# Kernel optimization log

Hardware: AMD Instinct MI355X
Metric: run time of the kernel (lower is better)

## Reference

```python
import jax, jax.numpy as jnp
import numpy as np

KS = 3
PAD = 1
N = KS * KS  # 9 sampling points per output location


def setup_inputs() -> dict:
    key = jax.random.key(0)
    k1, k2, k3 = jax.random.split(key, 3)
    b, c, H, W, outc = 4, 128, 64, 64, 128
    x = jax.random.normal(k1, (b, c, H, W), jnp.float32)
    offset = jax.random.normal(k2, (b, 2 * N, H, W), jnp.float32)
    weight = jax.random.normal(k3, (outc, c, KS, KS), jnp.float32) * 0.05
    return {"x": x, "offset": offset, "weight": weight}


def reference(x, offset, weight):
    b, c, H, W = x.shape
    h, w = offset.shape[2], offset.shape[3]
    # reorder interleaved (x,y,x,y,...) offset channels to (all x, all y)
    idx = jnp.concatenate([jnp.arange(0, 2 * N, 2), jnp.arange(1, 2 * N, 2)])
    offset = offset[:, idx]
    # zero padding
    xp = jnp.pad(x, ((0, 0), (0, 0), (PAD, PAD), (PAD, PAD)))
    Hp, Wp = H + 2 * PAD, W + 2 * PAD
    # kernel-relative offsets p_n: [1, 2N, 1, 1]
    r = np.arange(-(KS - 1) // 2, (KS - 1) // 2 + 1)
    pnx, pny = np.meshgrid(r, r, indexing='ij')
    p_n = jnp.asarray(np.concatenate([pnx.flatten(), pny.flatten()]).reshape(1, 2 * N, 1, 1), jnp.float32)
    # base grid p_0: [1, 2N, h, w], coords start at 1 (padded frame)
    p0x, p0y = np.meshgrid(np.arange(1, h + 1), np.arange(1, w + 1), indexing='ij')
    p_0 = jnp.asarray(np.concatenate([np.tile(p0x.reshape(1, 1, h, w), (1, N, 1, 1)),
                                      np.tile(p0y.reshape(1, 1, h, w), (1, N, 1, 1))], axis=1), jnp.float32)
    p = jnp.transpose(p_0 + p_n + offset, (0, 2, 3, 1))  # [b, h, w, 2N]
    px, py = p[..., :N], p[..., N:]
    fx, fy = jnp.floor(px), jnp.floor(py)
    # 4 corner integer coords, clamped to padded image
    q_lt_x = jnp.clip(fx, 0, Hp - 1).astype(jnp.int32)
    q_lt_y = jnp.clip(fy, 0, Wp - 1).astype(jnp.int32)
    q_rb_x = jnp.clip(fx + 1, 0, Hp - 1).astype(jnp.int32)
    q_rb_y = jnp.clip(fy + 1, 0, Wp - 1).astype(jnp.int32)
    # out-of-range mask: snap p to floor(p) there (matches original, incl. zero grad thru floor)
    mask_x = jax.lax.stop_gradient(((px < PAD) | (px > Hp - 1 - PAD)).astype(px.dtype))
    mask_y = jax.lax.stop_gradient(((py < PAD) | (py > Wp - 1 - PAD)).astype(py.dtype))
    px = px * (1 - mask_x) + fx * mask_x
    py = py * (1 - mask_y) + fy * mask_y
    px = jnp.clip(px, 0, Hp - 1)
    py = jnp.clip(py, 0, Wp - 1)
    qltx = q_lt_x.astype(px.dtype); qlty = q_lt_y.astype(px.dtype)
    qrbx = q_rb_x.astype(px.dtype); qrby = q_rb_y.astype(px.dtype)
    # bilinear weights: [b, h, w, N]
    g_lt = (1 + (qltx - px)) * (1 + (qlty - py))
    g_rb = (1 - (qrbx - px)) * (1 - (qrby - py))
    g_lb = (1 + (qltx - px)) * (1 - (qrby - py))
    g_rt = (1 - (qrbx - px)) * (1 + (qlty - py))

    xv = xp.reshape(b, c, Hp * Wp)

    def gather(qx, qy):
        lin = (qx * Wp + qy).reshape(b, 1, h * w * N)
        g = jnp.take_along_axis(xv, jnp.broadcast_to(lin, (b, c, h * w * N)), axis=2)
        return g.reshape(b, c, h, w, N)

    x_off = (g_lt[:, None] * gather(q_lt_x, q_lt_y)
             + g_rb[:, None] * gather(q_rb_x, q_rb_y)
             + g_lb[:, None] * gather(q_lt_x, q_rb_y)
             + g_rt[:, None] * gather(q_rb_x, q_lt_y))  # [b, c, h, w, N]
    # N = i*ks + j -> out[(h,i),(w,j)]
    xo = x_off.reshape(b, c, h, w, KS, KS).transpose(0, 1, 2, 4, 3, 5).reshape(b, c, h * KS, w * KS)
    out = jax.lax.conv_general_dilated(xo, weight, window_strides=(KS, KS), padding='VALID',
                                       dimension_numbers=('NCHW', 'OIHW', 'NCHW'))
    return out
```

## Files before the change

kernel.cpp:

```cpp
#include <hip/hip_runtime.h>


typedef __bf16  v8bf16 __attribute__((ext_vector_type(8)));
typedef __bf16  bf16x2 __attribute__((ext_vector_type(2)));
typedef float   f32x4  __attribute__((ext_vector_type(4)));
typedef float   f32x16 __attribute__((ext_vector_type(16)));
typedef unsigned short ushort4v __attribute__((ext_vector_type(4)));
typedef _Float16 half4v __attribute__((ext_vector_type(4)));

#define CIN  128
#define NPT  9
#define KTOT 1152
#define OC   128
#define PX   32
#define NDESC (NPT * PX)
#define KSTEPS 36
#define KSC  12
#define LDBc 392
#define KS32 72
#define KSC32 24
#define LDR32 392

#define PB_WFRAG 72
#define PB_XPOSE 1024
#define PB_TOTAL (PB_WFRAG + PB_XPOSE)

__device__ __forceinline__ uint4 desc_make(const float* __restrict__ off,
                                           int b, int i, int j, int tap) {
    float ox = off[(((b * 18) + 2 * tap) << 12) + (i << 6) + j];
    float oy = off[(((b * 18) + 2 * tap + 1) << 12) + (i << 6) + j];
    float px = (float)(i + tap / 3) + ox;
    float py = (float)(j + tap % 3) + oy;
    float fx = floorf(px), fy = floorf(py);
    int qltx = (int)fminf(fmaxf(fx, 0.f), 65.f);
    int qlty = (int)fminf(fmaxf(fy, 0.f), 65.f);
    int qrbx = (int)fminf(fmaxf(fx + 1.f, 0.f), 65.f);
    int qrby = (int)fminf(fmaxf(fy + 1.f, 0.f), 65.f);
    if (px < 1.f || px > 64.f) px = fx;
    if (py < 1.f || py > 64.f) py = fy;
    px = fminf(fmaxf(px, 0.f), 65.f);
    py = fminf(fmaxf(py, 0.f), 65.f);
    float wxl = 1.f + (float)qltx - px;
    float wxr = 1.f - ((float)qrbx - px);
    float wyl = 1.f + (float)qlty - py;
    float wyr = 1.f - ((float)qrby - py);
    float g[4] = { wxl * wyl, wxr * wyr, wxl * wyr, wxr * wyl };
    int qx[4] = { qltx, qrbx, qltx, qrbx };
    int qy[4] = { qlty, qrby, qrby, qlty };
    unsigned short idx[4];
    half4v gh;
    #pragma unroll
    for (int cr = 0; cr < 4; ++cr) {
        bool inb = (qx[cr] >= 1) && (qx[cr] <= 64) && (qy[cr] >= 1) && (qy[cr] <= 64);
        idx[cr] = inb ? (unsigned short)((qx[cr] - 1) * 64 + (qy[cr] - 1)) : 0;
        gh[cr]  = inb ? (_Float16)g[cr] : (_Float16)0.f;
    }
    uint4 rec;
    rec.x = (unsigned)idx[0] | ((unsigned)idx[1] << 16);
    rec.y = (unsigned)idx[2] | ((unsigned)idx[3] << 16);
    __builtin_memcpy(&rec.z, &gh, 8);
    return rec;
}

__global__ __launch_bounds__(256) void prep_kernel(
    const float* __restrict__ x, const float* __restrict__ w,
    __bf16* __restrict__ wfrag, __bf16* __restrict__ xt)
{
    __shared__ float tile[64][33];
    const int bid = blockIdx.x;
    const int tid = threadIdx.x;

    if (bid < PB_WFRAG) {
        int t = bid * 256 + tid;
        int lane = t & 63;
        int ks   = (t >> 6) % KS32;
        int ot4  = t / (KS32 * 64);
        int o    = ot4 * 32 + (lane & 31);
        v8bf16 frag;
        #pragma unroll
        for (int e = 0; e < 8; ++e) {
            int k   = ks * 16 + ((lane >> 5) * 8) + e;
            int tap = k >> 7, c = k & 127;
            frag[e] = (__bf16)w[(size_t)o * KTOT + c * NPT + tap];
        }
        *(v8bf16*)(wfrag + (size_t)t * 8) = frag;
    } else {
        const int bidx = bid - PB_WFRAG;
        const int b   = bidx >> 8;
        const int hw0 = ((bidx >> 2) & 63) * 64;
        const int c0  = (bidx & 3) * 32;
        #pragma unroll
        for (int r = 0; r < 8; ++r) {
            int c_l  = (tid >> 6) + r * 4;
            int hw_l = tid & 63;
            tile[hw_l][c_l] = x[((size_t)(b * CIN + c0 + c_l) << 12) + hw0 + hw_l];
        }
        __syncthreads();
        #pragma unroll
        for (int r = 0; r < 8; ++r) {
            int hw_l = (tid >> 5) + r * 8;
            int c_l  = tid & 31;
            xt[((size_t)(b * 4096 + hw0 + hw_l)) * CIN + c0 + c_l] = (__bf16)tile[hw_l][c_l];
        }
    }
}

__global__ __launch_bounds__(256) void fullk_kernel(
    const float* __restrict__ off, const __bf16* __restrict__ xt,
    const __bf16* __restrict__ wfrag, float* __restrict__ out)
{
    __shared__ __align__(16) __bf16 Bt[PX][LDR32];
    __shared__ __align__(16) uint4 sDesc[NDESC];

    const int bidx = blockIdx.x;
    const int b    = (bidx & 7) >> 1;
    const int sub  = ((bidx >> 3) << 1) | (bidx & 1);
    const int i    = sub >> 1;
    const int j0   = (sub & 1) * PX;
    const int tid  = threadIdx.x;

    const int l  = tid & 63;
    const int wv = tid >> 6;

    const __bf16* xtb = xt + (((size_t)b << 12) * CIN);

    {
        sDesc[tid] = desc_make(off, b, i, j0 + (tid & 31), tid >> 5);
        if (tid < 32) sDesc[256 + tid] = desc_make(off, b, i, j0 + tid, 8);
    }
    __syncthreads();

    f32x16 acc = {0.f,0.f,0.f,0.f,0.f,0.f,0.f,0.f,0.f,0.f,0.f,0.f,0.f,0.f,0.f,0.f};
    const __bf16* brow  = &Bt[l & 31][(l >> 5) * 8];
    const __bf16* warow = wfrag + (((size_t)wv * KS32) * 64 + l) * 8;

    const int q  = l >> 4;
    const int ll = l & 15;
    const __bf16* gbase = xtb + 8 * ll;

    for (int t = 0; t < 3; ++t) {
        {
            uint4 qd[6];
            int   pp[6], tt[6];
            #pragma unroll
            for (int m = 0; m < 6; ++m) {
                int dl = wv * 24 + m * 4 + q;
                tt[m] = dl >> 5;
                pp[m] = dl & 31;
                qd[m] = sDesc[t * 96 + dl];
            }

            #pragma unroll
            for (int h = 0; h < 2; ++h) {
                uint4  v[3][4];
                half4v gh[3];
                #pragma unroll
                for (int m = 0; m < 3; ++m) {
                    uint4 qm = qd[h * 3 + m];
                    unsigned int zz[2] = { qm.z, qm.w };
                    __builtin_memcpy(&gh[m], &zz, 8);
                    unsigned short idx[4] = {
                        (unsigned short)(qm.x & 0xffff), (unsigned short)(qm.x >> 16),
                        (unsigned short)(qm.y & 0xffff), (unsigned short)(qm.y >> 16) };
                    #pragma unroll
                    for (int cr = 0; cr < 4; ++cr)
                        v[m][cr] = *(const uint4*)(gbase + (size_t)idx[cr] * CIN);
                }
                #pragma unroll
                for (int m = 0; m < 3; ++m) {
                    float s[8] = {0.f,0.f,0.f,0.f,0.f,0.f,0.f,0.f};
                    #pragma unroll
                    for (int cr = 0; cr < 4; ++cr) {
                        float gf = (float)gh[m][cr];
                        unsigned int dw[4] = { v[m][cr].x, v[m][cr].y, v[m][cr].z, v[m][cr].w };
                        #pragma unroll
                        for (int e = 0; e < 4; ++e) {
                            float clo, chi;
                            unsigned int lo = dw[e] << 16, hi = dw[e] & 0xffff0000u;
                            __builtin_memcpy(&clo, &lo, 4);
                            __builtin_memcpy(&chi, &hi, 4);
                            s[2 * e]     += gf * clo;
                            s[2 * e + 1] += gf * chi;
                        }
                    }
                    v8bf16 pr;
                    #pragma unroll
                    for (int e = 0; e < 8; ++e) pr[e] = (__bf16)s[e];
                    int mm = h * 3 + m;
                    *(v8bf16*)&Bt[pp[mm]][tt[mm] * CIN + 8 * ll] = pr;
                }
            }
        }
        __syncthreads();

        #pragma unroll 6
        for (int ks = 0; ks < KSC32; ++ks) {
            v8bf16 afrag = *(const v8bf16*)(warow + (size_t)(t * KSC32 + ks) * 64 * 8);
            v8bf16 bfrag = *(const v8bf16*)(brow + ks * 16);
            acc = __builtin_amdgcn_mfma_f32_32x32x16_bf16(afrag, bfrag, acc, 0, 0, 0);
        }
        if (t < 2) __syncthreads();
    }

    {
        int obase = wv * 32 + 4 * (l >> 5);
        float* opb = out + (((size_t)(b * OC + obase)) << 12) + (i << 6) + j0 + (l & 31);
        #pragma unroll
        for (int reg = 0; reg < 16; ++reg) {
            int oo = (reg & 3) + 8 * (reg >> 2);
            opb[(size_t)oo << 12] = acc[reg];
        }
    }
}

__global__ __launch_bounds__(512, 8) void deform_fused_kernel(
    const float* __restrict__ x, const float* __restrict__ off,
    const float* __restrict__ w, const __bf16* __restrict__ wfrag,
    const __bf16* __restrict__ xt, float* __restrict__ out, int mode)
{
    __shared__ __align__(16) __bf16 Bt[PX][LDBc];
    __shared__ __align__(8)  unsigned short sIdxP[NDESC][4];
    __shared__ __align__(8)  _Float16      sGP[NDESC][4];

    const int bidx = blockIdx.x;
    const int b   = bidx >> 8;
    const int i   = (bidx >> 2) & 63;
    const int j0  = ((bidx >> 1) & 1) * PX;
    const int oh  = bidx & 1;
    const int tid = threadIdx.x;

    if (tid < NDESC) {
        int k = tid >> 5, p = tid & 31;
        int j = j0 + p;
        float ox = off[(((b * 18) + 2 * k) * 64 + i) * 64 + j];
        float oy = off[(((b * 18) + 2 * k + 1) * 64 + i) * 64 + j];
        float px = (float)(i + k / 3) + ox;
        float py = (float)(j + k % 3) + oy;
        float fx = floorf(px), fy = floorf(py);
        int qltx = (int)fminf(fmaxf(fx, 0.f), 65.f);
        int qlty = (int)fminf(fmaxf(fy, 0.f), 65.f);
        int qrbx = (int)fminf(fmaxf(fx + 1.f, 0.f), 65.f);
        int qrby = (int)fminf(fmaxf(fy + 1.f, 0.f), 65.f);
        if (px < 1.f || px > 64.f) px = fx;
        if (py < 1.f || py > 64.f) py = fy;
        px = fminf(fmaxf(px, 0.f), 65.f);
        py = fminf(fmaxf(py, 0.f), 65.f);
        float wxl = 1.f + (float)qltx - px;
        float wxr = 1.f - ((float)qrbx - px);
        float wyl = 1.f + (float)qlty - py;
        float wyr = 1.f - ((float)qrby - py);
        float g[4] = { wxl * wyl, wxr * wyr, wxl * wyr, wxr * wyl };
        int qx[4] = { qltx, qrbx, qltx, qrbx };
        int qy[4] = { qlty, qrby, qrby, qlty };
        #pragma unroll
        for (int cr = 0; cr < 4; ++cr) {
            bool inb = (qx[cr] >= 1) && (qx[cr] <= 64) && (qy[cr] >= 1) && (qy[cr] <= 64);
            sIdxP[tid][cr] = inb ? (unsigned short)((qx[cr] - 1) * 64 + (qy[cr] - 1)) : 0;
            sGP[tid][cr]   = inb ? (_Float16)g[cr] : (_Float16)0.f;
        }
    }
    __syncthreads();

    const int l    = tid & 63;
    const int wv   = tid >> 6;
    const int ot   = oh * 4 + (wv & 3);
    const int ph   = wv >> 2;
    const int quad = l >> 4;
    const int lr   = l & 15;

    f32x4 acc = {0.f, 0.f, 0.f, 0.f};
    const __bf16* xtb = xt + ((size_t)b * 4096) * CIN;
    const float*  xb  = x + ((size_t)b * CIN << 12);
    const __bf16* brow = &Bt[ph * 16 + lr][quad * 8];

    for (int t = 0; t < 3; ++t) {
        if (mode == 2) {
            #pragma unroll 4
            for (int dd = 0; dd < KSC; ++dd) {
                int dl = wv * KSC + dd;
                int tap_l = dl >> 5, p = dl & 31;
                int d = t * 96 + dl;
                ushort4v id = *(const ushort4v*)&sIdxP[d][0];
                half4v   gh = *(const half4v*)&sGP[d][0];
                float s0 = 0.f, s1 = 0.f;
                #pragma unroll
                for (int cr = 0; cr < 4; ++cr) {
                    unsigned int v = *(const unsigned int*)(xtb + (size_t)id[cr] * CIN + 2 * l);
                    float c0v, c1v;
                    unsigned int lo = v << 16, hi = v & 0xffff0000u;
                    __builtin_memcpy(&c0v, &lo, 4);
                    __builtin_memcpy(&c1v, &hi, 4);
                    float gf = (float)gh[cr];
                    s0 += gf * c0v;
                    s1 += gf * c1v;
                }
                bf16x2 pr = { (__bf16)s0, (__bf16)s1 };
                *(bf16x2*)&Bt[p][tap_l * CIN + 2 * l] = pr;
            }
        } else {
            for (int dd = 0; dd < KSC; ++dd) {
                int dl = wv * KSC + dd;
                int tap_l = dl >> 5, p = dl & 31;
                int d = t * 96 + dl;
                ushort4v id = *(const ushort4v*)&sIdxP[d][0];
                half4v   gh = *(const half4v*)&sGP[d][0];
                float s0 = 0.f, s1 = 0.f;
                #pragma unroll
                for (int cr = 0; cr < 4; ++cr) {
                    float gf = (float)gh[cr];
                    s0 += gf * xb[((size_t)(2 * l) << 12) + id[cr]];
                    s1 += gf * xb[((size_t)(2 * l + 1) << 12) + id[cr]];
                }
                bf16x2 pr = { (__bf16)s0, (__bf16)s1 };
                *(bf16x2*)&Bt[p][tap_l * CIN + 2 * l] = pr;
            }
        }
        __syncthreads();

        #pragma unroll 4
        for (int ks = 0; ks < KSC; ++ks) {
            int ks_g = t * KSC + ks;
            v8bf16 bfrag = *(const v8bf16*)(brow + ks * 32);
            v8bf16 afrag;
            if (mode >= 1) {
                afrag = *(const v8bf16*)(wfrag + (((size_t)ot * KSTEPS + ks_g) * 64 + l) * 8);
            } else {
                int o = ot * 16 + lr;
                #pragma unroll
                for (int e = 0; e < 8; ++e) {
                    int k = ks_g * 32 + quad * 8 + e;
                    int tap = k >> 7, c = k & 127;
                    afrag[e] = (__bf16)w[(size_t)o * KTOT + c * NPT + tap];
                }
            }
            acc = __builtin_amdgcn_mfma_f32_16x16x32_bf16(afrag, bfrag, acc, 0, 0, 0);
        }
        if (t < 2) __syncthreads();
    }

    {
        int obase = ot * 16 + quad * 4;
        float* op = out + (((size_t)(b * OC + obase)) << 12) + (i << 6) + j0 + ph * 16 + lr;
        #pragma unroll
        for (int r = 0; r < 4; ++r)
            op[(size_t)r << 12] = acc[r];
    }
}

__global__ __launch_bounds__(256) void wfrag_kernel(const float* __restrict__ w,
                                                    __bf16* __restrict__ wfrag) {
    int t = blockIdx.x * 256 + threadIdx.x;
    if (t >= 8 * KSTEPS * 64) return;
    int lane = t & 63;
    int ks   = (t >> 6) % KSTEPS;
    int ot   = t / (KSTEPS * 64);
    int o    = ot * 16 + (lane & 15);
    v8bf16 frag;
    #pragma unroll
    for (int e = 0; e < 8; ++e) {
        int k   = ks * 32 + (lane >> 4) * 8 + e;
        int tap = k >> 7, c = k & 127;
        frag[e] = (__bf16)w[(size_t)o * KTOT + c * NPT + tap];
    }
    *(v8bf16*)(wfrag + (size_t)t * 8) = frag;
}

__global__ __launch_bounds__(256) void xpose_kernel(const float* __restrict__ x,
                                                    __bf16* __restrict__ xt) {
    __shared__ float tile[64][33];
    const int bidx = blockIdx.x;
    const int b   = bidx >> 8;
    const int hw0 = ((bidx >> 2) & 63) * 64;
    const int c0  = (bidx & 3) * 32;
    const int tid = threadIdx.x;
    #pragma unroll
    for (int r = 0; r < 8; ++r) {
        int c_l  = (tid >> 6) + r * 4;
        int hw_l = tid & 63;
        tile[hw_l][c_l] = x[((size_t)(b * CIN + c0 + c_l) << 12) + hw0 + hw_l];
    }
    __syncthreads();
    #pragma unroll
    for (int r = 0; r < 8; ++r) {
        int hw_l = (tid >> 5) + r * 8;
        int c_l  = tid & 31;
        xt[((size_t)(b * 4096 + hw0 + hw_l)) * CIN + c0 + c_l] = (__bf16)tile[hw_l][c_l];
    }
}

extern "C" void kernel_launch(void* const* d_in, const int* in_sizes, int n_in,
                              void* d_out, int out_size, void* d_ws, size_t ws_size,
                              hipStream_t stream) {
    const float* x   = (const float*)d_in[0];
    const float* off = (const float*)d_in[1];
    const float* w   = (const float*)d_in[2];
    float* out = (float*)d_out;

    const size_t wfrag_bytes = (size_t)OC * KTOT * sizeof(__bf16);
    const size_t xt_bytes    = (size_t)4 * 4096 * CIN * sizeof(__bf16);

    int mode = 0;
    if (ws_size >= wfrag_bytes + xt_bytes) mode = 3;
    else if (ws_size >= wfrag_bytes) mode = 1;

    __bf16* wfrag = (__bf16*)d_ws;
    __bf16* xt    = (__bf16*)((char*)d_ws + wfrag_bytes);

    if (mode == 3) {
        prep_kernel<<<PB_TOTAL, 256, 0, stream>>>(x, w, wfrag, xt);
        fullk_kernel<<<512, 256, 0, stream>>>(off, xt, wfrag, out);
    } else {
        if (mode >= 1)
            wfrag_kernel<<<(8 * KSTEPS * 64 + 255) / 256, 256, 0, stream>>>(w, wfrag);
        deform_fused_kernel<<<4 * 64 * 2 * 2, 512, 0, stream>>>(x, off, w, wfrag, xt, out, mode);
    }
}
```

Before: 84.75 us.

## Switch fullk path to fp16 with packed-half blend and double-buffered B tile

Converts the prepared weights and transposed input to fp16 and uses fp16 MFMA. The bilinear blend now runs as packed half8 multiply-adds instead of unpacking bf16 to fp32. The B tile in shared memory is double-buffered, so the gather for the next tap group is issued before the MFMA loop on the current one, and launch bounds now request 2 blocks per CU. Accumulating the blend in fp16 lowers precision and risks overflow relative to fp32 accumulation, and the doubled shared memory buffer may limit occupancy.

Measured after the change: 83.88 us, median of 2. Within noise of the previous version (-1.0%).

```diff
diff --git a/kernel.cpp b/kernel.cpp
--- a/kernel.cpp
+++ b/kernel.cpp
@@ -7,6 +7,7 @@
 typedef float   f32x16 __attribute__((ext_vector_type(16)));
 typedef unsigned short ushort4v __attribute__((ext_vector_type(4)));
 typedef _Float16 half4v __attribute__((ext_vector_type(4)));
+typedef _Float16 half8  __attribute__((ext_vector_type(8)));
 
 #define CIN  128
 #define NPT  9
@@ -64,7 +65,7 @@
 
 __global__ __launch_bounds__(256) void prep_kernel(
     const float* __restrict__ x, const float* __restrict__ w,
-    __bf16* __restrict__ wfrag, __bf16* __restrict__ xt)
+    _Float16* __restrict__ wfrag, _Float16* __restrict__ xt)
 {
     __shared__ float tile[64][33];
     const int bid = blockIdx.x;
@@ -76,14 +77,14 @@
         int ks   = (t >> 6) % KS32;
         int ot4  = t / (KS32 * 64);
         int o    = ot4 * 32 + (lane & 31);
-        v8bf16 frag;
+        half8 frag;
         #pragma unroll
         for (int e = 0; e < 8; ++e) {
             int k   = ks * 16 + ((lane >> 5) * 8) + e;
             int tap = k >> 7, c = k & 127;
-            frag[e] = (__bf16)w[(size_t)o * KTOT + c * NPT + tap];
-        }
-        *(v8bf16*)(wfrag + (size_t)t * 8) = frag;
+            frag[e] = (_Float16)w[(size_t)o * KTOT + c * NPT + tap];
+        }
+        *(half8*)(wfrag + (size_t)t * 8) = frag;
     } else {
         const int bidx = bid - PB_WFRAG;
         const int b   = bidx >> 8;
@@ -100,16 +101,16 @@
         for (int r = 0; r < 8; ++r) {
             int hw_l = (tid >> 5) + r * 8;
             int c_l  = tid & 31;
-            xt[((size_t)(b * 4096 + hw0 + hw_l)) * CIN + c0 + c_l] = (__bf16)tile[hw_l][c_l];
-        }
-    }
-}
-
-__global__ __launch_bounds__(256) void fullk_kernel(
-    const float* __restrict__ off, const __bf16* __restrict__ xt,
-    const __bf16* __restrict__ wfrag, float* __restrict__ out)
+            xt[((size_t)(b * 4096 + hw0 + hw_l)) * CIN + c0 + c_l] = (_Float16)tile[hw_l][c_l];
+        }
+    }
+}
+
+__global__ __launch_bounds__(256, 2) void fullk_kernel(
+    const float* __restrict__ off, const _Float16* __restrict__ xt,
+    const _Float16* __restrict__ wfrag, float* __restrict__ out)
 {
-    __shared__ __align__(16) __bf16 Bt[PX][LDR32];
+    __shared__ __align__(16) _Float16 Bt[2][PX][LDR32];
     __shared__ __align__(16) uint4 sDesc[NDESC];
 
     const int bidx = blockIdx.x;
@@ -122,7 +123,7 @@
     const int l  = tid & 63;
     const int wv = tid >> 6;
 
-    const __bf16* xtb = xt + (((size_t)b << 12) * CIN);
+    const _Float16* xtb = xt + (((size_t)b << 12) * CIN);
 
     {
         sDesc[tid] = desc_make(off, b, i, j0 + (tid & 31), tid >> 5);
@@ -131,73 +132,65 @@
     __syncthreads();
 
     f32x16 acc = {0.f,0.f,0.f,0.f,0.f,0.f,0.f,0.f,0.f,0.f,0.f,0.f,0.f,0.f,0.f,0.f};
-    const __bf16* brow  = &Bt[l & 31][(l >> 5) * 8];
-    const __bf16* warow = wfrag + (((size_t)wv * KS32) * 64 + l) * 8;
+    const _Float16* warow = wfrag + (((size_t)wv * KS32) * 64 + l) * 8;
 
     const int q  = l >> 4;
     const int ll = l & 15;
-    const __bf16* gbase = xtb + 8 * ll;
+    const _Float16* gbase = xtb + 8 * ll;
+
+    auto stage = [&](int t, _Float16 (*B)[LDR32]) {
+        uint4 qd[6];
+        int   pp[6], tt[6];
+        #pragma unroll
+        for (int m = 0; m < 6; ++m) {
+            int dl = wv * 24 + m * 4 + q;
+            tt[m] = dl >> 5;
+            pp[m] = dl & 31;
+            qd[m] = sDesc[t * 96 + dl];
+        }
+        #pragma unroll
+        for (int h = 0; h < 2; ++h) {
+            uint4  v[3][4];
+            half4v gh[3];
+            #pragma unroll
+            for (int m = 0; m < 3; ++m) {
+                uint4 qm = qd[h * 3 + m];
+                unsigned int zz[2] = { qm.z, qm.w };
+                __builtin_memcpy(&gh[m], &zz, 8);
+                unsigned short idx[4] = {
+                    (unsigned short)(qm.x & 0xffff), (unsigned short)(qm.x >> 16),
+                    (unsigned short)(qm.y & 0xffff), (unsigned short)(qm.y >> 16) };
+                #pragma unroll
+                for (int cr = 0; cr < 4; ++cr)
+                    v[m][cr] = *(const uint4*)(gbase + (size_t)idx[cr] * CIN);
+            }
+            #pragma unroll
+            for (int m = 0; m < 3; ++m) {
+                half8 s = {0, 0, 0, 0, 0, 0, 0, 0};
+                #pragma unroll
+                for (int cr = 0; cr < 4; ++cr) {
+                    half8 vh;
+                    __builtin_memcpy(&vh, &v[m][cr], 16);
+                    s += vh * gh[m][cr];
+                }
+                int mm = h * 3 + m;
+                *(half8*)&B[pp[mm]][tt[mm] * CIN + 8 * ll] = s;
+            }
+        }
+    };
+
+    stage(0, Bt[0]);
+    __syncthreads();
 
     for (int t = 0; t < 3; ++t) {
-        {
-            uint4 qd[6];
-            int   pp[6], tt[6];
-            #pragma unroll
-            for (int m = 0; m < 6; ++m) {
-                int dl = wv * 24 + m * 4 + q;
-                tt[m] = dl >> 5;
-                pp[m] = dl & 31;
-                qd[m] = sDesc[t * 96 + dl];
-            }
-
-            #pragma unroll
-            for (int h = 0; h < 2; ++h) {
-                uint4  v[3][4];
-                half4v gh[3];
-                #pragma unroll
-                for (int m = 0; m < 3; ++m) {
-                    uint4 qm = qd[h * 3 + m];
-                    unsigned int zz[2] = { qm.z, qm.w };
-                    __builtin_memcpy(&gh[m], &zz, 8);
-                    unsigned short idx[4] = {
-                        (unsigned short)(qm.x & 0xffff), (unsigned short)(qm.x >> 16),
-                        (unsigned short)(qm.y & 0xffff), (unsigned short)(qm.y >> 16) };
-                    #pragma unroll
-                    for (int cr = 0; cr < 4; ++cr)
-                        v[m][cr] = *(const uint4*)(gbase + (size_t)idx[cr] * CIN);
-                }
-                #pragma unroll
-                for (int m = 0; m < 3; ++m) {
-                    float s[8] = {0.f,0.f,0.f,0.f,0.f,0.f,0.f,0.f};
-                    #pragma unroll
-                    for (int cr = 0; cr < 4; ++cr) {
-                        float gf = (float)gh[m][cr];
-                        unsigned int dw[4] = { v[m][cr].x, v[m][cr].y, v[m][cr].z, v[m][cr].w };
-                        #pragma unroll
-                        for (int e = 0; e < 4; ++e) {
-                            float clo, chi;
-                            unsigned int lo = dw[e] << 16, hi = dw[e] & 0xffff0000u;
-                            __builtin_memcpy(&clo, &lo, 4);
-                            __builtin_memcpy(&chi, &hi, 4);
-                            s[2 * e]     += gf * clo;
-                            s[2 * e + 1] += gf * chi;
-                        }
-                    }
-                    v8bf16 pr;
-                    #pragma unroll
-                    for (int e = 0; e < 8; ++e) pr[e] = (__bf16)s[e];
-                    int mm = h * 3 + m;
-                    *(v8bf16*)&Bt[pp[mm]][tt[mm] * CIN + 8 * ll] = pr;
-                }
-            }
-        }
-        __syncthreads();
-
+        if (t < 2) stage(t + 1, Bt[(t + 1) & 1]);
+
+        const _Float16* brow = &Bt[t & 1][l & 31][(l >> 5) * 8];
         #pragma unroll 6
         for (int ks = 0; ks < KSC32; ++ks) {
-            v8bf16 afrag = *(const v8bf16*)(warow + (size_t)(t * KSC32 + ks) * 64 * 8);
-            v8bf16 bfrag = *(const v8bf16*)(brow + ks * 16);
-            acc = __builtin_amdgcn_mfma_f32_32x32x16_bf16(afrag, bfrag, acc, 0, 0, 0);
+            half8 afrag = *(const half8*)(warow + (size_t)(t * KSC32 + ks) * 64 * 8);
+            half8 bfrag = *(const half8*)(brow + ks * 16);
+            acc = __builtin_amdgcn_mfma_f32_32x32x16_f16(afrag, bfrag, acc, 0, 0, 0);
         }
         if (t < 2) __syncthreads();
     }
@@ -396,20 +389,21 @@
     const float* w   = (const float*)d_in[2];
     float* out = (float*)d_out;
 
-    const size_t wfrag_bytes = (size_t)OC * KTOT * sizeof(__bf16);
-    const size_t xt_bytes    = (size_t)4 * 4096 * CIN * sizeof(__bf16);
+    const size_t wfrag_bytes = (size_t)OC * KTOT * 2;
+    const size_t xt_bytes    = (size_t)4 * 4096 * CIN * 2;
 
     int mode = 0;
     if (ws_size >= wfrag_bytes + xt_bytes) mode = 3;
     else if (ws_size >= wfrag_bytes) mode = 1;
 
-    __bf16* wfrag = (__bf16*)d_ws;
-    __bf16* xt    = (__bf16*)((char*)d_ws + wfrag_bytes);
-
     if (mode == 3) {
+        _Float16* wfrag = (_Float16*)d_ws;
+        _Float16* xt    = (_Float16*)((char*)d_ws + wfrag_bytes);
         prep_kernel<<<PB_TOTAL, 256, 0, stream>>>(x, w, wfrag, xt);
         fullk_kernel<<<512, 256, 0, stream>>>(off, xt, wfrag, out);
     } else {
+        __bf16* wfrag = (__bf16*)d_ws;
+        __bf16* xt    = (__bf16*)((char*)d_ws + wfrag_bytes);
         if (mode >= 1)
             wfrag_kernel<<<(8 * KSTEPS * 64 + 255) / 256, 256, 0, stream>>>(w, wfrag);
         deform_fused_kernel<<<4 * 64 * 2 * 2, 512, 0, stream>>>(x, off, w, wfrag, xt, out, mode);
```
